# Kernel tuning notes

Measured on AMD Instinct MI355X. Metric: run time of the kernel, lower is better.

## Reference

```python
import jax, jax.numpy as jnp
import numpy as np

N = 512
BATCH = 128
EPS = 1e-08


def setup_inputs() -> dict:
    key = jax.random.key(0)
    kx, kb = jax.random.split(key)
    # binary indicator of which items are present in each set
    x = jax.random.randint(kx, (BATCH, N), 0, 2, dtype=jnp.int32)
    # column-normalized random feature matrix, as in the torch __init__
    B = jax.random.normal(kb, (N, N), dtype=jnp.float32)
    B = B / jnp.linalg.norm(B, axis=0, keepdims=True)
    return {"x": x, "B": B}


def reference(x, B):
    n = B.shape[0]
    I = jnp.eye(n, dtype=B.dtype)
    L = B.T @ B + EPS * I                      # (n, n) PSD kernel
    m = (x != 0).astype(B.dtype)               # (batch, n) active-item mask
    # zero out rows and cols of inactive items, put 1 on their diagonal
    Lb = L[None, :, :] * m[:, :, None] * m[:, None, :]   # (batch, n, n)
    Lb = Lb + I[None, :, :] * (1.0 - m)[:, None, :]
    _, logdet_b = jnp.linalg.slogdet(Lb)       # (batch,)
    _, logdet_Z = jnp.linalg.slogdet(L + I)    # scalar normalizer
    return logdet_b - logdet_Z
```

## Files before the change

kernel.cpp:

```cpp
#include <hip/hip_runtime.h>
#include <math.h>

#define N 512
#define BATCH 128
#define EPS 1e-8f
#define TPB 1024
#define NW 16
#define KP 304
#define LN2 0.69314718055994530942f
#define SPLIT 144
#define GSTR 152
#define SLD2 372

typedef _Float16 f16;
typedef _Float16 f16x8 __attribute__((ext_vector_type(8)));
typedef float f32x4 __attribute__((ext_vector_type(4)));

__device__ __forceinline__ int lh_base(int r) {
    const int a = r >> 3, b = r & 7;
    return 8 * (a + 1) * (4 * a + b);
}

#define G1_OFF 22016
#define ARENA_SZ 159744
#define SLAB_BYTES (368 * SLD2 * 4)

__device__ __forceinline__ float rdl(float v, int l) {
    return __builtin_bit_cast(float,
        __builtin_amdgcn_readlane(__builtin_bit_cast(int, v), l));
}

__device__ __forceinline__ void tri_map(int e, int* r_out, int* c_out) {
    int rr = (int)((sqrtf(8.0f * (float)e + 1.0f) - 1.0f) * 0.5f);
    while ((((rr + 1) * (rr + 2)) >> 1) <= e) ++rr;
    while (((rr * (rr + 1)) >> 1) > e) --rr;
    *r_out = rr;
    *c_out = e - ((rr * (rr + 1)) >> 1);
}

__global__ __launch_bounds__(256) void compute_L(const float* __restrict__ B,
                                                 float* __restrict__ L) {
    const int r0 = blockIdx.x * 64, c0 = blockIdx.y * 64;
    const int tx = threadIdx.x & 15, ty = threadIdx.x >> 4;
    __shared__ float Bi[16][64];
    __shared__ float Bj[16][64];
    float acc[4][4] = {};
    for (int k0 = 0; k0 < N; k0 += 16) {
#pragma unroll
        for (int q = 0; q < 4; ++q) {
            const int e = threadIdx.x + q * 256;
            const int kr = e >> 6, cc = e & 63;
            Bi[kr][cc] = B[(k0 + kr) * N + r0 + cc];
            Bj[kr][cc] = B[(k0 + kr) * N + c0 + cc];
        }
        __syncthreads();
#pragma unroll
        for (int kq = 0; kq < 16; ++kq) {
            float a[4], b[4];
#pragma unroll
            for (int q = 0; q < 4; ++q) {
                a[q] = Bi[kq][ty * 4 + q];
                b[q] = Bj[kq][tx * 4 + q];
            }
#pragma unroll
            for (int i = 0; i < 4; ++i)
#pragma unroll
                for (int j = 0; j < 4; ++j) acc[i][j] = fmaf(a[i], b[j], acc[i][j]);
        }
        __syncthreads();
    }
#pragma unroll
    for (int i = 0; i < 4; ++i) {
        const int r = r0 + ty * 4 + i;
        f32x4 v;
#pragma unroll
        for (int j = 0; j < 4; ++j) {
            const int c = c0 + tx * 4 + j;
            v[j] = acc[i][j] + ((r == c) ? EPS : 0.0f);
        }
        *(f32x4*)(&L[r * N + c0 + tx * 4]) = v;
    }
}

template <int MODE>
__device__ __forceinline__ float gath(const float* __restrict__ L,
                                      const float* __restrict__ S, const short* idx,
                                      int k, bool add1, int gr, int gc) {
    if constexpr (MODE <= 1) {
        if (gr < k && gc < k) {
            float v = L[(int)idx[gr] * N + (int)idx[gc]];
            if (add1 && gr == gc) v += 1.0f;
            return v;
        }
        return (gr == gc) ? 1.0f : 0.0f;
    } else {
        if (gr < k && gc < k) {
            const int r2 = gr > gc ? gr : gc, c2 = gr > gc ? gc : gr;
            return S[r2 * SLD2 + c2];
        }
        return (gr == gc) ? 1.0f : 0.0f;
    }
}

template <int MODE, int CT>
__device__ float chol_panels(char* arena, const float* __restrict__ S,
                             const float* __restrict__ L, const short* idx,
                             int k, int rows, int ncols, bool add1) {
    const int tid = threadIdx.x;
    const int lane = tid & 63, wv = tid >> 6;
    constexpr int p_off = (MODE == 0) ? 94848 : (MODE == 1) ? 133888 : 138368;
    constexpr int m_off = (MODE == 0) ? 119424 : (MODE == 1) ? 158464 : 156032;
    f16* Lh = (f16*)arena;
    f16* Gl = (f16*)(arena + G1_OFF);
    f16* P = (f16*)(arena + p_off);
    f16* M = (f16*)(arena + m_off);
    const int frow = lane & 15, koff = (lane >> 4) * 8;
    const int crow = (lane >> 4) * 4, ccol = lane & 15;

    float lg2 = 0.0f;
    const int npan = ncols >> 4;
    for (int p = 0; p < npan; ++p) {
        const int jb = p << 4;
        const int ntile = (rows - jb) >> 4;

        int r0_[CT], baseA_[CT];
        bool val_[CT], isg_[CT];
#pragma unroll
        for (int it = 0; it < CT; ++it) {
            const int ti = (wv == 0) ? (it == 0 ? 0 : (1 << 20)) : (wv + 15 * it);
            const bool v = ti < ntile;
            const int r0 = jb + ((v ? ti : 0) << 4);
            r0_[it] = r0;
            val_[it] = v;
            const bool gg = (MODE == 1) && v && (r0 >= SPLIT);
            isg_[it] = gg;
            baseA_[it] = gg ? ((r0 - SPLIT + frow) * GSTR + koff)
                            : (lh_base(r0 + frow) + koff);
        }
        const int baseB = lh_base(jb + frow) + koff;

        f32x4 g_[CT];
#pragma unroll
        for (int it = 0; it < CT; ++it)
            if (val_[it]) {
#pragma unroll
                for (int q = 0; q < 4; ++q)
                    g_[it][q] = gath<MODE>(L, S, idx, k, add1, r0_[it] + crow + q, jb + ccol);
            }

        const int nkk = (jb + 31) >> 5;
        f32x4 acc_[CT];
#pragma unroll
        for (int it = 0; it < CT; ++it) acc_[it] = (f32x4){0.f, 0.f, 0.f, 0.f};

        for (int cg = 0; cg < nkk; cg += 4) {
            f16x8 A_[4][CT], B_[4];
#pragma unroll
            for (int u = 0; u < 4; ++u) {
                const int c = cg + u;
                const int kk = c << 5;
                const bool ok = (c < nkk) && (kk + koff < jb);
                B_[u] = ok ? *(const f16x8*)(&Lh[baseB + kk]) : (f16x8){};
#pragma unroll
                for (int it = 0; it < CT; ++it) {
                    f16x8 vv = {};
                    if (ok && val_[it]) {
                        if (MODE == 1 && isg_[it]) vv = *(const f16x8*)(&Gl[baseA_[it] + kk]);
                        else vv = *(const f16x8*)(&Lh[baseA_[it] + kk]);
                    }
                    A_[u][it] = vv;
                }
            }
#pragma unroll
            for (int u = 0; u < 4; ++u) {
                if (cg + u < nkk) {
#pragma unroll
                    for (int it = 0; it < CT; ++it)
                        if (val_[it])
                            acc_[it] = __builtin_amdgcn_mfma_f32_16x16x32_f16(
                                A_[u][it], B_[u], acc_[it], 0, 0, 0);
                }
            }
        }

#pragma unroll
        for (int it = 0; it < CT; ++it)
            if (val_[it]) {
                const int lr = r0_[it] - jb;
#pragma unroll
                for (int q = 0; q < 4; ++q)
                    P[(lr + crow + q) * 24 + ccol] = (f16)(g_[it][q] - acc_[it][q]);
            }

        f16x8 afs[CT];
#pragma unroll
        for (int it = 0; it < CT; ++it) {
            f16x8 af = {};
            if (val_[it] && wv != 0 && koff < 16) {
                const int lr = r0_[it] - jb;
                af = *(const f16x8*)(&P[(lr + frow) * 24 + koff]);
            }
            afs[it] = af;
        }

        if (wv == 0) {
            const int r = lane & 15;
            float row[16], w[16];
#pragma unroll
            for (int c = 0; c < 16; ++c) row[c] = (float)P[r * 24 + c];
#pragma unroll
            for (int c = 0; c < 16; ++c) w[c] = (c == r) ? 1.0f : 0.0f;
#pragma unroll
            for (int j = 0; j < 16; ++j) {
                const float piv = rdl(row[j], j);
                lg2 += __log2f(piv);
                const float irs = rsqrtf(piv);
                row[j] *= irs;
                w[j] *= irs;
#pragma unroll
                for (int cc = j + 1; cc < 16; ++cc) {
                    const float s = rdl(row[j], cc);
                    row[cc] = fmaf(-row[j], s, row[cc]);
                    w[cc] = fmaf(-s, w[j], w[cc]);
                }
            }
            if (lane < 16) {
                f16x8 hv0, hv1;
#pragma unroll
                for (int m = 0; m < 8; ++m) {
                    hv0[m] = (f16)row[m];
                    hv1[m] = (f16)row[8 + m];
                }
                *(f16x8*)(&Lh[lh_base(jb + lane) + jb]) = hv0;
                if (lane >= 8) *(f16x8*)(&Lh[lh_base(jb + lane) + jb + 8]) = hv1;
            }
            if (lane < 32) {
#pragma unroll
                for (int i = 0; i < 16; ++i)
                    M[i * 40 + lane] = (lane < 16) ? (f16)w[i] : (f16)0.0f;
            }
        }
        __syncthreads();

        const f16x8 bfM = *(const f16x8*)(&M[frow * 40 + koff]);
#pragma unroll
        for (int it = 0; it < CT; ++it) {
            if (val_[it] && wv != 0) {
                f32x4 xx = {0.f, 0.f, 0.f, 0.f};
                xx = __builtin_amdgcn_mfma_f32_16x16x32_f16(afs[it], bfM, xx, 0, 0, 0);
#pragma unroll
                for (int q = 0; q < 4; ++q) {
                    const int gr = r0_[it] + crow + q;
                    const f16 h = (f16)xx[q];
                    if (MODE == 1 && gr >= SPLIT) Gl[(gr - SPLIT) * GSTR + jb + ccol] = h;
                    else Lh[lh_base(gr) + jb + ccol] = h;
                }
            }
        }
        __syncthreads();
    }
    return lg2;
}

__device__ void schur_gemm(char* arena, float* __restrict__ S,
                           const float* __restrict__ L, const short* idx,
                           int k, int k2p, bool add1) {
    const int tid = threadIdx.x;
    const int lane = tid & 63, wv = tid >> 6;
    const f16* Gl = (const f16*)(arena + G1_OFF);
    const int frow = lane & 15, koff = (lane >> 4) * 8;
    const int crow = (lane >> 4) * 4, ccol = lane & 15;
    const int nt2 = k2p >> 4, TT = (nt2 * (nt2 + 1)) >> 1;
    const int nkk = (SPLIT + 31) >> 5;
    for (int e = wv; e < TT; e += NW) {
        int R, C;
        tri_map(e, &R, &C);
        const int r0 = R << 4, c0 = C << 4;
        f32x4 g;
#pragma unroll
        for (int q = 0; q < 4; ++q) {
            const int gr = SPLIT + r0 + crow + q, gc = SPLIT + c0 + ccol;
            float v;
            if (gr < k && gc < k) {
                v = L[(int)idx[gr] * N + (int)idx[gc]];
                if (add1 && gr == gc) v += 1.0f;
            } else v = (gr == gc) ? 1.0f : 0.0f;
            g[q] = v;
        }
        const int ba = (r0 + frow) * GSTR + koff, bb = (c0 + frow) * GSTR + koff;
        f32x4 acc = {0.f, 0.f, 0.f, 0.f};
        for (int cg = 0; cg < nkk; cg += 4) {
            f16x8 A_[4], B_[4];
#pragma unroll
            for (int u = 0; u < 4; ++u) {
                const int c = cg + u, kk = c << 5;
                const bool ok = (c < nkk) && (kk + koff < SPLIT);
                A_[u] = ok ? *(const f16x8*)(&Gl[ba + kk]) : (f16x8){};
                B_[u] = ok ? *(const f16x8*)(&Gl[bb + kk]) : (f16x8){};
            }
#pragma unroll
            for (int u = 0; u < 4; ++u)
                if (cg + u < nkk)
                    acc = __builtin_amdgcn_mfma_f32_16x16x32_f16(A_[u], B_[u], acc, 0, 0, 0);
        }
#pragma unroll
        for (int q = 0; q < 4; ++q)
            S[(r0 + crow + q) * SLD2 + c0 + ccol] = g[q] - acc[q];
    }
}

__global__ __launch_bounds__(TPB, 4) void chol_all(const int* __restrict__ x,
                                                   const float* __restrict__ L,
                                                   char* __restrict__ slabs, int nslabs,
                                                   float* __restrict__ logs) {
    const int b = blockIdx.x;
    const int tid = threadIdx.x;
    const int lane = tid & 63, wv = tid >> 6;
    __shared__ __align__(16) char arena[ARENA_SZ];
    __shared__ short idx[N];
    __shared__ int wcnt[NW];

    const bool zc = (b == BATCH);
    const bool inx = tid < N;
    const bool act = zc ? inx : (inx && x[(size_t)b * N + tid] != 0);
    const unsigned long long m = __ballot(act);
    if (lane == 0) wcnt[wv] = __popcll(m);
    __syncthreads();
    int off = 0, ktot = 0;
    for (int q = 0; q < NW; ++q) {
        if (q < wv) off += wcnt[q];
        ktot += wcnt[q];
    }
    if (act) idx[off + __popcll(m & ((1ULL << lane) - 1ULL))] = (short)tid;
    __syncthreads();

    const int k = ktot;
    const int kp = (k + 15) & ~15;

    float lg2;
    if (!zc && kp <= KP) {
        lg2 = chol_panels<0, 2>(arena, nullptr, L, idx, k, kp, kp, false);
    } else {
        const int si = zc ? 0 : (nslabs > 1 ? 1 + (b % (nslabs - 1)) : 0);
        float* S = (float*)(slabs + (size_t)si * SLAB_BYTES);
        const int k2 = k - SPLIT, k2p = kp - SPLIT;
        lg2 = chol_panels<1, 3>(arena, nullptr, L, idx, k, kp, SPLIT, zc);
        schur_gemm(arena, S, L, idx, k, k2p, zc);
        __syncthreads();
        lg2 += chol_panels<2, 2>(arena, S, L, idx, k2, k2p, k2p, false);
    }
    if (tid == 0) logs[b] = lg2 * LN2;
}

__global__ void finalize(const float* __restrict__ logs, float* __restrict__ out) {
    const int i = threadIdx.x;
    out[i] = logs[i] - logs[BATCH];
}

extern "C" void kernel_launch(void* const* d_in, const int* in_sizes, int n_in,
                              void* d_out, int out_size, void* d_ws, size_t ws_size,
                              hipStream_t stream) {
    const int* x = (const int*)d_in[0];
    const float* B = (const float*)d_in[1];
    float* out = (float*)d_out;

    char* ws = (char*)d_ws;
    const size_t L_bytes = (size_t)N * N * 4;
    float* L = (float*)ws;
    float* logs = (float*)(ws + L_bytes);
    const size_t head = L_bytes + 4096;
    char* slabs = ws + head;
    int nslabs = (ws_size > head) ? (int)((ws_size - head) / SLAB_BYTES) : 1;
    if (nslabs < 1) nslabs = 1;
    if (nslabs > 9) nslabs = 9;

    compute_L<<<dim3(8, 8), 256, 0, stream>>>(B, L);
    chol_all<<<BATCH + 1, TPB, 0, stream>>>(x, L, slabs, nslabs, logs);
    finalize<<<1, BATCH, 0, stream>>>(logs, out);
}
```

Baseline: 178.7 us.

## Factor two 16-wide panels per step to halve block barriers in Cholesky

Restructures the blocked Cholesky so each outer step handles a 32-column panel. Wave 0 factors both 16x16 diagonal blocks and the coupling block in sequence, while the other waves update their two column tiles with an intra-step correction. This halves the number of __syncthreads-separated panel steps and raises the SPLIT point to 160, with the shared-memory arena and slab strides re-laid out to match. The cost is more serial work on wave 0 per step and higher register use.

```diff
diff --git a/kernel.cpp b/kernel.cpp
--- a/kernel.cpp
+++ b/kernel.cpp
@@ -8,9 +8,10 @@
 #define NW 16
 #define KP 304
 #define LN2 0.69314718055994530942f
-#define SPLIT 144
-#define GSTR 152
-#define SLD2 372
+#define SPLIT 160
+#define GSTR 160
+#define SLD2 356
+#define SLAB_BYTES (352 * SLD2 * 4)
 
 typedef _Float16 f16;
 typedef _Float16 f16x8 __attribute__((ext_vector_type(8)));
@@ -21,9 +22,14 @@
     return 8 * (a + 1) * (4 * a + b);
 }
 
-#define G1_OFF 22016
-#define ARENA_SZ 159744
-#define SLAB_BYTES (368 * SLD2 * 4)
+#define G1_OFF   26880
+#define SCR0_OFF 94848
+#define M0_OFF   113280
+#define SCR1_OFF 139520
+#define M1_OFF   157952
+#define SCR2_OFF 126720
+#define M2_OFF   145152
+#define ARENA_SZ 160512
 
 __device__ __forceinline__ float rdl(float v, int l) {
     return __builtin_bit_cast(float,
@@ -102,176 +108,239 @@
     }
 }
 
-template <int MODE, int CT>
-__device__ float chol_panels(char* arena, const float* __restrict__ S,
-                             const float* __restrict__ L, const short* idx,
-                             int k, int rows, int ncols, bool add1) {
+template <int MODE>
+__device__ float chol32(char* arena, const float* __restrict__ S,
+                        const float* __restrict__ L, const short* idx,
+                        int k, int rows, int ncols, bool add1) {
     const int tid = threadIdx.x;
     const int lane = tid & 63, wv = tid >> 6;
-    constexpr int p_off = (MODE == 0) ? 94848 : (MODE == 1) ? 133888 : 138368;
-    constexpr int m_off = (MODE == 0) ? 119424 : (MODE == 1) ? 158464 : 156032;
+    constexpr int scr_off = (MODE == 0) ? SCR0_OFF : (MODE == 1) ? SCR1_OFF : SCR2_OFF;
+    constexpr int m_off = (MODE == 0) ? M0_OFF : (MODE == 1) ? M1_OFF : M2_OFF;
     f16* Lh = (f16*)arena;
     f16* Gl = (f16*)(arena + G1_OFF);
-    f16* P = (f16*)(arena + p_off);
-    f16* M = (f16*)(arena + m_off);
+    f16* scr = (f16*)(arena + scr_off) + wv * 576;
+    f16* Mm = (f16*)(arena + m_off);
     const int frow = lane & 15, koff = (lane >> 4) * 8;
     const int crow = (lane >> 4) * 4, ccol = lane & 15;
+    const f32x4 zz = {0.f, 0.f, 0.f, 0.f};
 
     float lg2 = 0.0f;
-    const int npan = ncols >> 4;
-    for (int p = 0; p < npan; ++p) {
-        const int jb = p << 4;
+
+    auto ld_af = [&]() -> f16x8 {
+        if (koff < 16) return *(const f16x8*)(&scr[frow * 36 + koff]);
+        f16x8 z = {};
+        return z;
+    };
+    auto scr_st = [&](const f32x4& v) {
+#pragma unroll
+        for (int q = 0; q < 4; ++q) scr[(crow + q) * 36 + ccol] = (f16)v[q];
+    };
+    auto factor16 = [&](int rbase, int cbase, f16* mdst) {
+        float row[16], w[16];
+#pragma unroll
+        for (int c = 0; c < 16; ++c) row[c] = (float)scr[frow * 36 + c];
+#pragma unroll
+        for (int c = 0; c < 16; ++c) w[c] = (c == frow) ? 1.0f : 0.0f;
+#pragma unroll
+        for (int j = 0; j < 16; ++j) {
+            const float piv = rdl(row[j], j);
+            lg2 += __log2f(piv);
+            const float irs = rsqrtf(piv);
+            row[j] *= irs;
+            w[j] *= irs;
+#pragma unroll
+            for (int cc = j + 1; cc < 16; ++cc) {
+                const float s2 = rdl(row[j], cc);
+                row[cc] = fmaf(-row[j], s2, row[cc]);
+                w[cc] = fmaf(-s2, w[j], w[cc]);
+            }
+        }
+        if (lane < 16) {
+            f16x8 hv0, hv1;
+#pragma unroll
+            for (int m2 = 0; m2 < 8; ++m2) {
+                hv0[m2] = (f16)row[m2];
+                hv1[m2] = (f16)row[8 + m2];
+            }
+            *(f16x8*)(&Lh[lh_base(rbase + lane) + cbase]) = hv0;
+            if (lane >= 8) *(f16x8*)(&Lh[lh_base(rbase + lane) + cbase + 8]) = hv1;
+        }
+        if (lane < 32) {
+#pragma unroll
+            for (int i = 0; i < 16; ++i)
+                mdst[i * 40 + lane] = (lane < 16) ? (f16)w[i] : (f16)0.0f;
+        }
+    };
+    auto stX = [&](const f32x4& x, int rr0, int cb) {
+#pragma unroll
+        for (int q = 0; q < 4; ++q) {
+            const int gr = rr0 + crow + q;
+            const f16 h = (f16)x[q];
+            if (MODE == 1 && gr >= SPLIT) Gl[(gr - SPLIT) * GSTR + cb + ccol] = h;
+            else Lh[lh_base(gr) + cb + ccol] = h;
+        }
+    };
+
+    for (int jb = 0; jb < ncols; jb += 32) {
+        const bool half = (ncols - jb) <= 16;
+        const int nkk = jb >> 5;
         const int ntile = (rows - jb) >> 4;
-
-        int r0_[CT], baseA_[CT];
-        bool val_[CT], isg_[CT];
-#pragma unroll
-        for (int it = 0; it < CT; ++it) {
-            const int ti = (wv == 0) ? (it == 0 ? 0 : (1 << 20)) : (wv + 15 * it);
-            const bool v = ti < ntile;
-            const int r0 = jb + ((v ? ti : 0) << 4);
-            r0_[it] = r0;
-            val_[it] = v;
-            const bool gg = (MODE == 1) && v && (r0 >= SPLIT);
-            isg_[it] = gg;
-            baseA_[it] = gg ? ((r0 - SPLIT + frow) * GSTR + koff)
-                            : (lh_base(r0 + frow) + koff);
-        }
-        const int baseB = lh_base(jb + frow) + koff;
-
-        f32x4 g_[CT];
-#pragma unroll
-        for (int it = 0; it < CT; ++it)
-            if (val_[it]) {
+        const int nbelow = ntile - (half ? 1 : 2);
+        const int rb0 = jb + (half ? 16 : 32);
+
+        bool val_[2] = {false, false};
+        int r0_[2] = {0, 0};
+        f16x8 afs_[2] = {};
+        f32x4 s1_[2] = {};
+
+        if (wv == 0) {
+            f32x4 g00 = zz, g10 = zz, g11 = zz;
+#pragma unroll
+            for (int q = 0; q < 4; ++q)
+                g00[q] = gath<MODE>(L, S, idx, k, add1, jb + crow + q, jb + ccol);
+            if (!half) {
+#pragma unroll
+                for (int q = 0; q < 4; ++q) {
+                    g10[q] = gath<MODE>(L, S, idx, k, add1, jb + 16 + crow + q, jb + ccol);
+                    g11[q] = gath<MODE>(L, S, idx, k, add1, jb + 16 + crow + q, jb + 16 + ccol);
+                }
+            }
+            const int bF0 = lh_base(jb + frow) + koff;
+            const int bF1 = lh_base(jb + 16 + frow) + koff;
+            f32x4 a00 = zz, a10 = zz, a11 = zz;
+            for (int c = 0; c < nkk; ++c) {
+                const int kk = c << 5;
+                const f16x8 F0 = *(const f16x8*)(&Lh[bF0 + kk]);
+                a00 = __builtin_amdgcn_mfma_f32_16x16x32_f16(F0, F0, a00, 0, 0, 0);
+                if (!half) {
+                    const f16x8 F1 = *(const f16x8*)(&Lh[bF1 + kk]);
+                    a10 = __builtin_amdgcn_mfma_f32_16x16x32_f16(F1, F0, a10, 0, 0, 0);
+                    a11 = __builtin_amdgcn_mfma_f32_16x16x32_f16(F1, F1, a11, 0, 0, 0);
+                }
+            }
+            f32x4 s00;
+#pragma unroll
+            for (int q = 0; q < 4; ++q) s00[q] = g00[q] - a00[q];
+            scr_st(s00);
+            factor16(jb, jb, Mm);
+            if (!half) {
+                f32x4 s10;
+#pragma unroll
+                for (int q = 0; q < 4; ++q) s10[q] = g10[q] - a10[q];
+                scr_st(s10);
+                const f16x8 af10 = ld_af();
+                const f16x8 bM0 = *(const f16x8*)(&Mm[frow * 40 + koff]);
+                const f32x4 x10 = __builtin_amdgcn_mfma_f32_16x16x32_f16(af10, bM0, zz, 0, 0, 0);
 #pragma unroll
                 for (int q = 0; q < 4; ++q)
-                    g_[it][q] = gath<MODE>(L, S, idx, k, add1, r0_[it] + crow + q, jb + ccol);
-            }
-
-        const int nkk = (jb + 31) >> 5;
-        f32x4 acc_[CT];
-#pragma unroll
-        for (int it = 0; it < CT; ++it) acc_[it] = (f32x4){0.f, 0.f, 0.f, 0.f};
-
-        for (int cg = 0; cg < nkk; cg += 4) {
-            f16x8 A_[4][CT], B_[4];
-#pragma unroll
-            for (int u = 0; u < 4; ++u) {
-                const int c = cg + u;
+                    Lh[lh_base(jb + 16 + crow + q) + jb + ccol] = (f16)x10[q];
+                scr_st(x10);
+                const f16x8 afx = ld_af();
+                const f32x4 pr = __builtin_amdgcn_mfma_f32_16x16x32_f16(afx, afx, zz, 0, 0, 0);
+                f32x4 s11;
+#pragma unroll
+                for (int q = 0; q < 4; ++q) s11[q] = g11[q] - a11[q] - pr[q];
+                scr_st(s11);
+                factor16(jb + 16, jb + 16, Mm + 640);
+            }
+        } else {
+            bool isg_[2];
+            int baseA_[2];
+#pragma unroll
+            for (int it = 0; it < 2; ++it) {
+                const int tb = (wv - 1) + 15 * it;
+                val_[it] = tb < nbelow;
+                const int rr = rb0 + 16 * (val_[it] ? tb : 0);
+                r0_[it] = rr;
+                isg_[it] = (MODE == 1) && val_[it] && (rr >= SPLIT);
+                baseA_[it] = isg_[it] ? ((rr - SPLIT + frow) * GSTR + koff)
+                                      : (lh_base(rr + frow) + koff);
+            }
+            f32x4 g0_[2] = {zz, zz}, g1_[2] = {zz, zz};
+#pragma unroll
+            for (int it = 0; it < 2; ++it)
+                if (val_[it]) {
+#pragma unroll
+                    for (int q = 0; q < 4; ++q) {
+                        g0_[it][q] = gath<MODE>(L, S, idx, k, add1, r0_[it] + crow + q, jb + ccol);
+                        if (!half)
+                            g1_[it][q] = gath<MODE>(L, S, idx, k, add1, r0_[it] + crow + q, jb + 16 + ccol);
+                    }
+                }
+            const int bB0 = lh_base(jb + frow) + koff;
+            const int bB1 = lh_base(jb + 16 + frow) + koff;
+            f32x4 ac0_[2] = {zz, zz}, ac1_[2] = {zz, zz};
+            for (int c = 0; c < nkk; ++c) {
                 const int kk = c << 5;
-                const bool ok = (c < nkk) && (kk + koff < jb);
-                B_[u] = ok ? *(const f16x8*)(&Lh[baseB + kk]) : (f16x8){};
-#pragma unroll
-                for (int it = 0; it < CT; ++it) {
-                    f16x8 vv = {};
-                    if (ok && val_[it]) {
-                        if (MODE == 1 && isg_[it]) vv = *(const f16x8*)(&Gl[baseA_[it] + kk]);
-                        else vv = *(const f16x8*)(&Lh[baseA_[it] + kk]);
+                const f16x8 B0 = *(const f16x8*)(&Lh[bB0 + kk]);
+                f16x8 B1 = {};
+                if (!half) B1 = *(const f16x8*)(&Lh[bB1 + kk]);
+#pragma unroll
+                for (int it = 0; it < 2; ++it)
+                    if (val_[it]) {
+                        const f16x8 A = isg_[it] ? *(const f16x8*)(&Gl[baseA_[it] + kk])
+                                                 : *(const f16x8*)(&Lh[baseA_[it] + kk]);
+                        ac0_[it] = __builtin_amdgcn_mfma_f32_16x16x32_f16(A, B0, ac0_[it], 0, 0, 0);
+                        if (!half)
+                            ac1_[it] = __builtin_amdgcn_mfma_f32_16x16x32_f16(A, B1, ac1_[it], 0, 0, 0);
                     }
-                    A_[u][it] = vv;
+            }
+#pragma unroll
+            for (int it = 0; it < 2; ++it)
+                if (val_[it]) {
+                    f32x4 s0;
+#pragma unroll
+                    for (int q = 0; q < 4; ++q) s0[q] = g0_[it][q] - ac0_[it][q];
+                    scr_st(s0);
+                    afs_[it] = ld_af();
+                    if (!half) {
+#pragma unroll
+                        for (int q = 0; q < 4; ++q) s1_[it][q] = g1_[it][q] - ac1_[it][q];
+                    }
                 }
-            }
-#pragma unroll
-            for (int u = 0; u < 4; ++u) {
-                if (cg + u < nkk) {
-#pragma unroll
-                    for (int it = 0; it < CT; ++it)
-                        if (val_[it])
-                            acc_[it] = __builtin_amdgcn_mfma_f32_16x16x32_f16(
-                                A_[u][it], B_[u], acc_[it], 0, 0, 0);
+        }
+        __syncthreads();
+
+        {
+            const f16x8 bM0 = *(const f16x8*)(&Mm[frow * 40 + koff]);
+            f16x8 bM1 = {}, bX10 = {};
+            if (!half) {
+                bM1 = *(const f16x8*)(&Mm[640 + frow * 40 + koff]);
+                bX10 = *(const f16x8*)(&Lh[lh_base(jb + 16 + frow) + jb + koff]);
+            }
+#pragma unroll
+            for (int it = 0; it < 2; ++it)
+                if (val_[it]) {
+                    const f32x4 x0 = __builtin_amdgcn_mfma_f32_16x16x32_f16(afs_[it], bM0, zz, 0, 0, 0);
+                    stX(x0, r0_[it], jb);
+                    if (!half) {
+                        scr_st(x0);
+                        const f16x8 afx = ld_af();
+                        const f32x4 pr = __builtin_amdgcn_mfma_f32_16x16x32_f16(afx, bX10, zz, 0, 0, 0);
+                        f32x4 s1p;
+#pragma unroll
+                        for (int q = 0; q < 4; ++q) s1p[q] = s1_[it][q] - pr[q];
+                        scr_st(s1p);
+                        const f16x8 af1 = ld_af();
+                        const f32x4 x1 = __builtin_amdgcn_mfma_f32_16x16x32_f16(af1, bM1, zz, 0, 0, 0);
+                        stX(x1, r0_[it], jb + 16);
+                    }
                 }
-            }
-        }
-
-#pragma unroll
-        for (int it = 0; it < CT; ++it)
-            if (val_[it]) {
-                const int lr = r0_[it] - jb;
-#pragma unroll
-                for (int q = 0; q < 4; ++q)
-                    P[(lr + crow + q) * 24 + ccol] = (f16)(g_[it][q] - acc_[it][q]);
-            }
-
-        f16x8 afs[CT];
-#pragma unroll
-        for (int it = 0; it < CT; ++it) {
-            f16x8 af = {};
-            if (val_[it] && wv != 0 && koff < 16) {
-                const int lr = r0_[it] - jb;
-                af = *(const f16x8*)(&P[(lr + frow) * 24 + koff]);
-            }
-            afs[it] = af;
-        }
-
-        if (wv == 0) {
-            const int r = lane & 15;
-            float row[16], w[16];
-#pragma unroll
-            for (int c = 0; c < 16; ++c) row[c] = (float)P[r * 24 + c];
-#pragma unroll
-            for (int c = 0; c < 16; ++c) w[c] = (c == r) ? 1.0f : 0.0f;
-#pragma unroll
-            for (int j = 0; j < 16; ++j) {
-                const float piv = rdl(row[j], j);
-                lg2 += __log2f(piv);
-                const float irs = rsqrtf(piv);
-                row[j] *= irs;
-                w[j] *= irs;
-#pragma unroll
-                for (int cc = j + 1; cc < 16; ++cc) {
-                    const float s = rdl(row[j], cc);
-                    row[cc] = fmaf(-row[j], s, row[cc]);
-                    w[cc] = fmaf(-s, w[j], w[cc]);
-                }
-            }
-            if (lane < 16) {
-                f16x8 hv0, hv1;
-#pragma unroll
-                for (int m = 0; m < 8; ++m) {
-                    hv0[m] = (f16)row[m];
-                    hv1[m] = (f16)row[8 + m];
-                }
-                *(f16x8*)(&Lh[lh_base(jb + lane) + jb]) = hv0;
-                if (lane >= 8) *(f16x8*)(&Lh[lh_base(jb + lane) + jb + 8]) = hv1;
-            }
-            if (lane < 32) {
-#pragma unroll
-                for (int i = 0; i < 16; ++i)
-                    M[i * 40 + lane] = (lane < 16) ? (f16)w[i] : (f16)0.0f;
-            }
         }
         __syncthreads();
-
-        const f16x8 bfM = *(const f16x8*)(&M[frow * 40 + koff]);
-#pragma unroll
-        for (int it = 0; it < CT; ++it) {
-            if (val_[it] && wv != 0) {
-                f32x4 xx = {0.f, 0.f, 0.f, 0.f};
-                xx = __builtin_amdgcn_mfma_f32_16x16x32_f16(afs[it], bfM, xx, 0, 0, 0);
-#pragma unroll
-                for (int q = 0; q < 4; ++q) {
-                    const int gr = r0_[it] + crow + q;
-                    const f16 h = (f16)xx[q];
-                    if (MODE == 1 && gr >= SPLIT) Gl[(gr - SPLIT) * GSTR + jb + ccol] = h;
-                    else Lh[lh_base(gr) + jb + ccol] = h;
-                }
-            }
-        }
-        __syncthreads();
     }
     return lg2;
 }
 
-__device__ void schur_gemm(char* arena, float* __restrict__ S,
-                           const float* __restrict__ L, const short* idx,
-                           int k, int k2p, bool add1) {
+__device__ void schur32(char* arena, float* __restrict__ S,
+                        const float* __restrict__ L, const short* idx,
+                        int k, int k2p, bool add1) {
     const int tid = threadIdx.x;
     const int lane = tid & 63, wv = tid >> 6;
     const f16* Gl = (const f16*)(arena + G1_OFF);
     const int frow = lane & 15, koff = (lane >> 4) * 8;
     const int crow = (lane >> 4) * 4, ccol = lane & 15;
     const int nt2 = k2p >> 4, TT = (nt2 * (nt2 + 1)) >> 1;
-    const int nkk = (SPLIT + 31) >> 5;
     for (int e = wv; e < TT; e += NW) {
         int R, C;
         tri_map(e, &R, &C);
@@ -289,19 +358,11 @@
         }
         const int ba = (r0 + frow) * GSTR + koff, bb = (c0 + frow) * GSTR + koff;
         f32x4 acc = {0.f, 0.f, 0.f, 0.f};
-        for (int cg = 0; cg < nkk; cg += 4) {
-            f16x8 A_[4], B_[4];
-#pragma unroll
-            for (int u = 0; u < 4; ++u) {
-                const int c = cg + u, kk = c << 5;
-                const bool ok = (c < nkk) && (kk + koff < SPLIT);
-                A_[u] = ok ? *(const f16x8*)(&Gl[ba + kk]) : (f16x8){};
-                B_[u] = ok ? *(const f16x8*)(&Gl[bb + kk]) : (f16x8){};
-            }
-#pragma unroll
-            for (int u = 0; u < 4; ++u)
-                if (cg + u < nkk)
-                    acc = __builtin_amdgcn_mfma_f32_16x16x32_f16(A_[u], B_[u], acc, 0, 0, 0);
+#pragma unroll
+        for (int c = 0; c < SPLIT / 32; ++c) {
+            const f16x8 A = *(const f16x8*)(&Gl[ba + (c << 5)]);
+            const f16x8 B = *(const f16x8*)(&Gl[bb + (c << 5)]);
+            acc = __builtin_amdgcn_mfma_f32_16x16x32_f16(A, B, acc, 0, 0, 0);
         }
 #pragma unroll
         for (int q = 0; q < 4; ++q)
@@ -339,15 +400,15 @@
 
     float lg2;
     if (!zc && kp <= KP) {
-        lg2 = chol_panels<0, 2>(arena, nullptr, L, idx, k, kp, kp, false);
+        lg2 = chol32<0>(arena, nullptr, L, idx, k, kp, kp, false);
     } else {
         const int si = zc ? 0 : (nslabs > 1 ? 1 + (b % (nslabs - 1)) : 0);
         float* S = (float*)(slabs + (size_t)si * SLAB_BYTES);
         const int k2 = k - SPLIT, k2p = kp - SPLIT;
-        lg2 = chol_panels<1, 3>(arena, nullptr, L, idx, k, kp, SPLIT, zc);
-        schur_gemm(arena, S, L, idx, k, k2p, zc);
+        lg2 = chol32<1>(arena, nullptr, L, idx, k, kp, SPLIT, zc);
+        schur32(arena, S, L, idx, k, k2p, zc);
         __syncthreads();
-        lg2 += chol_panels<2, 2>(arena, S, L, idx, k2, k2p, k2p, false);
+        lg2 += chol32<2>(arena, S, L, idx, k2, k2p, k2p, false);
     }
     if (tid == 0) logs[b] = lg2 * LN2;
 }
```

New measurement: 160.9 us (median of 2 runs). 1.11x faster.
